# Performance work log

Measured on AMD Instinct MI355X. Metric: run time of the kernel, lower is better.

The kernel has to match this reference:

```python
import jax, jax.numpy as jnp
import numpy as np


def _layernorm(x, g, b, eps=1e-5):
    m = x.mean(-1, keepdims=True)
    v = ((x - m) ** 2).mean(-1, keepdims=True)
    return (x - m) / jnp.sqrt(v + eps) * g + b


def _rotate_every_two(x):
    x1 = x[..., ::2]
    x2 = x[..., 1::2]
    return jnp.stack([-x2, x1], axis=-1).reshape(x.shape)


def _segsum(x):
    # x: (..., L) of negative decay rates -> (..., L, L) bidirectional segment sums
    cs = jnp.cumsum(x, axis=-1)
    d = cs[..., :, None] - cs[..., None, :]
    L = x.shape[-1]
    i = jnp.arange(L)[:, None]
    j = jnp.arange(L)[None, :]
    # lower-tri (incl diag): cs[i]-cs[j]; strict upper: cs[j]-cs[i]; diag is 0
    return jnp.where(i >= j, d, -d)


def _forward(x, y, th, dw1_w, dw1_b, dw2_w, dw2_b, qw, qb, kw, kb, vw, vb,
             lepe_w, lepe_b, dt_w, dt_bias, A_log, ow, ob,
             n1_g, n1_b, ffn_w1, ffn_b1, ffn_w2, ffn_b2, n2_g, n2_b):
    B, C, H, W = x.shape
    nh = dt_bias.shape[0]
    hd = C // nh
    scaling = hd ** (-0.5)

    # dynamic gated fusion of the two kv branches (1x1 convs == channel matmuls)
    fusion = jnp.concatenate([y, th], axis=1)                      # (B,2C,H,W)
    hid = jax.nn.relu(jnp.einsum('bchw,oc->bohw', fusion, dw1_w) + dw1_b[None, :, None, None])
    logits = jnp.einsum('bchw,oc->bohw', hid, dw2_w) + dw2_b[None, :, None, None]
    wts = jax.nn.softmax(logits, axis=1)                           # (B,2,H,W)
    fused = y * wts[:, 0:1] + th * wts[:, 1:2]

    xh = jnp.transpose(x, (0, 2, 3, 1))                            # (B,H,W,C)
    fkv = jnp.transpose(fused, (0, 2, 3, 1))

    # 2D RoPE tables (flattened raster index)
    angle = jnp.repeat(1.0 / 10000 ** jnp.linspace(0.0, 1.0, hd // 2), 2)
    idx = jnp.arange(H * W, dtype=x.dtype)
    sin = jnp.sin(idx[:, None] * angle[None, :]).reshape(H, W, hd)
    cos = jnp.cos(idx[:, None] * angle[None, :]).reshape(H, W, hd)

    q = xh @ qw + qb
    k = fkv @ kw + kb
    v = fkv @ vw + vb

    # depthwise 5x5 conv position term on v (NHWC)
    lepe = jax.lax.conv_general_dilated(
        v, lepe_w, (1, 1), ((2, 2), (2, 2)),
        dimension_numbers=('NHWC', 'HWIO', 'NHWC'), feature_group_count=C) + lepe_b

    k = k * scaling
    q = q.reshape(B, H, W, nh, hd).transpose(0, 3, 1, 2, 4)        # (B,nh,H,W,hd)
    k = k.reshape(B, H, W, nh, hd).transpose(0, 3, 1, 2, 4)
    v5 = v.reshape(B, H, W, nh, hd).transpose(0, 3, 1, 2, 4)

    qr = q * cos + _rotate_every_two(q) * sin
    kr = k * cos + _rotate_every_two(k) * sin

    # PathEmbeding2D: data-dependent decay masks
    xt = xh.reshape(B, H * W, nh, hd)
    dt = xt @ dt_w                                                 # (B,S,nh,2)
    A = -jnp.exp(A_log)                                            # (nh,)
    da = jax.nn.softplus(dt[..., 0] + dt_bias) * A                 # (B,S,nh)
    db = jax.nn.softplus(dt[..., 1] + dt_bias) * A
    mask_w = _segsum(da.reshape(B, H, W, nh).transpose(0, 1, 3, 2))  # (B,H,nh,W,W)
    mask_h = _segsum(db.reshape(B, H, W, nh).transpose(0, 2, 3, 1))  # (B,W,nh,H,H)

    # row (width-direction) and column (height-direction) attentions
    qk_w = jax.nn.softmax(jnp.einsum('bnhid,bnhjd->bhnij', qr, kr) + mask_w, axis=-1)  # (B,H,nh,W,W)
    qk_h = jax.nn.softmax(jnp.einsum('bnhwd,bngwd->bwnhg', qr, kr) + mask_h, axis=-1)  # (B,W,nh,H,H)

    v_w = jnp.einsum('bhnij,bnhjd->bhnid', qk_w, v5)               # (B,H,nh,W,hd)
    out1 = jnp.einsum('bwnhg,bgnwd->bwnhd', qk_h, v_w)             # (B,W,nh,H,hd)
    out1 = out1.transpose(0, 3, 1, 2, 4).reshape(B, H, W, C)

    v_h = jnp.einsum('bwnhg,bngwd->bwnhd', qk_h, v5)               # (B,W,nh,H,hd)
    out2 = jnp.einsum('bhnij,bjnhd->bhnid', qk_w, v_h)             # (B,H,nh,W,hd)
    out2 = out2.transpose(0, 1, 3, 2, 4).reshape(B, H, W, C)

    out = 0.5 * out1 + 0.5 * out2 + lepe
    out = out @ ow + ob
    out = _layernorm(xh + out, n1_g, n1_b)
    ffn = jax.nn.gelu(out @ ffn_w1 + ffn_b1, approximate=False) @ ffn_w2 + ffn_b2
    out = _layernorm(out + ffn, n2_g, n2_b)
    return jnp.transpose(out, (0, 3, 1, 2))                        # (B,C,H,W)


def setup_inputs() -> dict:
    B, C, H, W, nh = 4, 64, 128, 128, 4
    hd = C // nh
    key = jax.random.key(0)
    ks = jax.random.split(key, 20)
    n = lambda k, shp, s: jax.random.normal(k, shp, dtype=jnp.float32) * s
    rng = np.random.default_rng(0)
    dt = np.exp(rng.uniform(0.0, 1.0, nh) * (np.log(0.1) - np.log(0.001)) + np.log(0.001))
    dt = np.clip(dt, 1e-4, None)
    dt_bias = jnp.asarray(dt + np.log(-np.expm1(-dt)), dtype=jnp.float32)
    A_log = jnp.asarray(np.log(rng.uniform(1.0, 1.1, nh)), dtype=jnp.float32)
    inp = {
        'x': n(ks[0], (B, C, H, W), 1.0),
        'y': n(ks[1], (B, C, H, W), 1.0),
        'th': n(ks[2], (B, C, H, W), 1.0),
        'dw1_w': n(ks[3], (C, 2 * C), (2 * C) ** -0.5),
        'dw1_b': jnp.zeros((C,), jnp.float32),
        'dw2_w': n(ks[4], (2, C), C ** -0.5),
        'dw2_b': jnp.zeros((2,), jnp.float32),
        'qw': n(ks[5], (C, C), 0.2 * C ** -0.5),
        'qb': jnp.zeros((C,), jnp.float32),
        'kw': n(ks[6], (C, C), 0.2 * C ** -0.5),
        'kb': jnp.zeros((C,), jnp.float32),
        'vw': n(ks[7], (C, C), 0.2 * C ** -0.5),
        'vb': jnp.zeros((C,), jnp.float32),
        'lepe_w': n(ks[8], (5, 5, 1, C), 0.1),
        'lepe_b': jnp.zeros((C,), jnp.float32),
        'dt_w': n(ks[9], (hd, 2), hd ** -0.5),
        'dt_bias': dt_bias,
        'A_log': A_log,
        'ow': n(ks[10], (C, C), C ** -0.5),
        'ob': jnp.zeros((C,), jnp.float32),
        'n1_g': jnp.ones((C,), jnp.float32),
        'n1_b': jnp.zeros((C,), jnp.float32),
        'ffn_w1': n(ks[11], (C, 4 * C), C ** -0.5),
        'ffn_b1': jnp.zeros((4 * C,), jnp.float32),
        'ffn_w2': n(ks[12], (4 * C, C), (4 * C) ** -0.5),
        'ffn_b2': jnp.zeros((C,), jnp.float32),
        'n2_g': jnp.ones((C,), jnp.float32),
        'n2_b': jnp.zeros((C,), jnp.float32),
    }
    return inp


def reference(x, y, th, dw1_w, dw1_b, dw2_w, dw2_b, qw, qb, kw, kb, vw, vb,
              lepe_w, lepe_b, dt_w, dt_bias, A_log, ow, ob,
              n1_g, n1_b, ffn_w1, ffn_b1, ffn_w2, ffn_b2, n2_g, n2_b):
    return _forward(x, y, th, dw1_w, dw1_b, dw2_w, dw2_b, qw, qb, kw, kb, vw, vb,
                    lepe_w, lepe_b, dt_w, dt_bias, A_log, ow, ob,
                    n1_g, n1_b, ffn_w1, ffn_b1, ffn_w2, ffn_b2, n2_g, n2_b)
```

## Files before the change

kernel.cpp:

```cpp
#include <hip/hip_runtime.h>
#include <math.h>

#define HWSZ 16384

typedef __attribute__((ext_vector_type(8))) short bf16x8;
typedef __attribute__((ext_vector_type(4))) float f32x4;
typedef unsigned short u16;

union U4 { uint4 v; u16 s[8]; };
union U2 { uint2 v; u16 s[4]; };

__device__ __forceinline__ float gelu_f(float v) {
    return 0.5f * v * (1.0f + erff(v * 0.70710678118654752f));
}
__device__ __forceinline__ float splus_f(float v) {
    return (v > 20.f) ? v : log1pf(expf(v));
}
__device__ __forceinline__ u16 f2bf(float f) {
    union { float f; unsigned u; } v; v.f = f;
    unsigned r = (v.u + 0x7FFF + ((v.u >> 16) & 1)) >> 16;
    return (u16)r;
}
__device__ __forceinline__ unsigned pk2(float a, float b) {
    return (unsigned)f2bf(a) | ((unsigned)f2bf(b) << 16);
}
__device__ __forceinline__ float bf2f(u16 s) {
    union { unsigned u; float f; } v; v.u = ((unsigned)s) << 16; return v.f;
}

__global__ __launch_bounds__(256) void k_prep(
    const float* __restrict__ w1, const float* __restrict__ qw,
    const float* __restrict__ kw, const float* __restrict__ vw,
    const float* __restrict__ ow, const float* __restrict__ fw1s,
    const float* __restrict__ fw2s, u16* __restrict__ wout)
{
    int id = blockIdx.x*256 + threadIdx.x;
    float v;
    if (id < 8192) {
        v = w1[id];
    } else if (id < 20480) {
        int t = id - 8192; int m = t >> 12;
        int i = t & 4095; int o = i >> 6, c = i & 63;
        const float* src = (m==0) ? qw : ((m==1) ? kw : vw);
        v = src[c*64 + o];
        if (m == 1) v *= 0.25f;
    } else if (id < 24576) {
        int i = id - 20480; int c = i >> 6, k = i & 63;
        v = ow[k*64 + c];
    } else if (id < 40960) {
        int i = id - 24576; int o = i >> 6, k = i & 63;
        v = fw1s[k*256 + o];
    } else {
        int i = id - 40960; int jc = i >> 12; int r = i & 4095;
        int c = r >> 6, k2 = r & 63;
        v = fw2s[(jc*64 + k2)*64 + c];
    }
    wout[id] = f2bf(v);
}

#define FS 136
__global__ __launch_bounds__(256) void k_fuse(
    const float* __restrict__ y, const float* __restrict__ th,
    const u16* __restrict__ wfuse, const float* __restrict__ b1,
    const float* __restrict__ w2, const float* __restrict__ b2,
    u16* __restrict__ fused)
{
    __shared__ u16 Fsh[128*FS];
    __shared__ u16 Wt[64*FS];
    int tid = threadIdx.x, bid = blockIdx.x;
    int pbase = bid*128;
    int b = pbase >> 14, p0 = pbase & 16383;
    for (int vi = tid; vi < 1024; vi += 256) {
        int cp = vi >> 5;
        int p4 = (vi & 31)*4;
        int c0 = cp*2;
        float4 a = *(const float4*)&y [((size_t)(b*64+c0  ))*HWSZ + p0 + p4];
        float4 c = *(const float4*)&y [((size_t)(b*64+c0+1))*HWSZ + p0 + p4];
        *(unsigned*)&Fsh[(p4+0)*FS + c0] = pk2(a.x, c.x);
        *(unsigned*)&Fsh[(p4+1)*FS + c0] = pk2(a.y, c.y);
        *(unsigned*)&Fsh[(p4+2)*FS + c0] = pk2(a.z, c.z);
        *(unsigned*)&Fsh[(p4+3)*FS + c0] = pk2(a.w, c.w);
        float4 e = *(const float4*)&th[((size_t)(b*64+c0  ))*HWSZ + p0 + p4];
        float4 f = *(const float4*)&th[((size_t)(b*64+c0+1))*HWSZ + p0 + p4];
        *(unsigned*)&Fsh[(p4+0)*FS + 64 + c0] = pk2(e.x, f.x);
        *(unsigned*)&Fsh[(p4+1)*FS + 64 + c0] = pk2(e.y, f.y);
        *(unsigned*)&Fsh[(p4+2)*FS + 64 + c0] = pk2(e.z, f.z);
        *(unsigned*)&Fsh[(p4+3)*FS + 64 + c0] = pk2(e.w, f.w);
    }
    for (int vi = tid; vi < 1024; vi += 256) {
        int o = vi >> 4, s8 = (vi & 15)*8;
        *(uint4*)&Wt[o*FS + s8] = *(const uint4*)&wfuse[o*128 + s8];
    }
    __syncthreads();
    int lane = tid & 63, wv = tid >> 6;
    int quad = lane >> 4, lm = lane & 15;
    int M0 = wv*32;
    f32x4 z = {0.f,0.f,0.f,0.f};
    f32x4 acc[2][4];
    #pragma unroll
    for (int mt = 0; mt < 2; ++mt)
        #pragma unroll
        for (int nt = 0; nt < 4; ++nt) acc[mt][nt] = z;
    #pragma unroll
    for (int ks = 0; ks < 4; ++ks) {
        bf16x8 aF[2];
        #pragma unroll
        for (int mt = 0; mt < 2; ++mt)
            aF[mt] = *(bf16x8*)&Fsh[(M0+mt*16+lm)*FS + ks*32 + quad*8];
        #pragma unroll
        for (int nt = 0; nt < 4; ++nt) {
            bf16x8 bW = *(bf16x8*)&Wt[(nt*16+lm)*FS + ks*32 + quad*8];
            #pragma unroll
            for (int mt = 0; mt < 2; ++mt)
                acc[mt][nt] = __builtin_amdgcn_mfma_f32_16x16x32_bf16(aF[mt], bW, acc[mt][nt], 0,0,0);
        }
    }
    float b1v[4], w2av[4], w2bv[4];
    #pragma unroll
    for (int nt = 0; nt < 4; ++nt) {
        int o = nt*16 + lm;
        b1v[nt] = b1[o]; w2av[nt] = w2[o]; w2bv[nt] = w2[64+o];
    }
    float bias2a = b2[0], bias2b = b2[1];
    size_t gbase = (size_t)(b*16384 + p0);
    #pragma unroll
    for (int mt = 0; mt < 2; ++mt) {
        #pragma unroll
        for (int r = 0; r < 4; ++r) {
            int p = M0 + mt*16 + quad*4 + r;
            float l0 = 0.f, l1 = 0.f;
            #pragma unroll
            for (int nt = 0; nt < 4; ++nt) {
                float h = fmaxf(acc[mt][nt][r] + b1v[nt], 0.f);
                l0 += h * w2av[nt];
                l1 += h * w2bv[nt];
            }
            l0 += __shfl_xor(l0,1,64); l0 += __shfl_xor(l0,2,64);
            l0 += __shfl_xor(l0,4,64); l0 += __shfl_xor(l0,8,64);
            l1 += __shfl_xor(l1,1,64); l1 += __shfl_xor(l1,2,64);
            l1 += __shfl_xor(l1,4,64); l1 += __shfl_xor(l1,8,64);
            l0 += bias2a; l1 += bias2b;
            float m = fmaxf(l0, l1);
            float e0 = __expf(l0 - m), e1 = __expf(l1 - m);
            float inv = 1.f/(e0 + e1);
            float wa = e0*inv, wb = e1*inv;
            U2 yv, tv;
            yv.v = *(uint2*)&Fsh[p*FS + lm*4];
            tv.v = *(uint2*)&Fsh[p*FS + 64 + lm*4];
            unsigned o0 = pk2(bf2f(yv.s[0])*wa + bf2f(tv.s[0])*wb,
                              bf2f(yv.s[1])*wa + bf2f(tv.s[1])*wb);
            unsigned o1 = pk2(bf2f(yv.s[2])*wa + bf2f(tv.s[2])*wb,
                              bf2f(yv.s[3])*wa + bf2f(tv.s[3])*wb);
            *(uint2*)&fused[(gbase + p)*64 + lm*4] = make_uint2(o0, o1);
        }
    }
}

__global__ __launch_bounds__(256) void k_qkv(
    const float* __restrict__ x, const u16* __restrict__ fused,
    const u16* __restrict__ bq, const float* __restrict__ qb,
    const u16* __restrict__ bk, const float* __restrict__ kb,
    const u16* __restrict__ bv, const float* __restrict__ vb,
    const float* __restrict__ dtw, const float* __restrict__ dtb,
    const float* __restrict__ alog,
    u16* __restrict__ qr, u16* __restrict__ kr, u16* __restrict__ v5,
    float* __restrict__ da, float* __restrict__ db)
{
    __shared__ u16 Ax[64*72];
    __shared__ u16 Af[64*72];
    __shared__ u16 Bq[64*72], Bk[64*72], Bv[64*72];
    int tid = threadIdx.x, bid = blockIdx.x;
    int pbase = bid*64;
    int b = pbase >> 14, p0 = pbase & 16383;
    for (int vi = tid; vi < 512; vi += 256) {
        int cp = vi >> 4, p4 = (vi & 15)*4;
        int c0 = cp*2;
        float4 a = *(const float4*)&x[((size_t)(b*64+c0  ))*HWSZ + p0 + p4];
        float4 c = *(const float4*)&x[((size_t)(b*64+c0+1))*HWSZ + p0 + p4];
        *(unsigned*)&Ax[(p4+0)*72 + c0] = pk2(a.x, c.x);
        *(unsigned*)&Ax[(p4+1)*72 + c0] = pk2(a.y, c.y);
        *(unsigned*)&Ax[(p4+2)*72 + c0] = pk2(a.z, c.z);
        *(unsigned*)&Ax[(p4+3)*72 + c0] = pk2(a.w, c.w);
    }
    for (int vi = tid; vi < 512; vi += 256) {
        int p = vi >> 3, seg = (vi & 7)*8;
        *(uint4*)&Af[p*72 + seg] = *(const uint4*)&fused[((size_t)(b*16384) + p0 + p)*64 + seg];
    }
    for (int vi = tid; vi < 1536; vi += 256) {
        int m = vi >> 9;
        int i = vi & 511;
        int o = i >> 3, s8 = (i & 7)*8;
        const u16* src = (m==0) ? bq : ((m==1) ? bk : bv);
        u16* dst = (m==0) ? Bq : ((m==1) ? Bk : Bv);
        *(uint4*)&dst[o*72 + s8] = *(const uint4*)&src[o*64 + s8];
    }
    __syncthreads();
    int lane = tid & 63, wv = tid >> 6;
    int quad = lane >> 4, lm = lane & 15;
    int M0 = wv*16;
    f32x4 z = {0.f,0.f,0.f,0.f};
    f32x4 accQ[4], accK[4], accV[4];
    #pragma unroll
    for (int nt = 0; nt < 4; ++nt) { accQ[nt]=z; accK[nt]=z; accV[nt]=z; }
    #pragma unroll
    for (int ks = 0; ks < 2; ++ks) {
        bf16x8 aX = *(bf16x8*)&Ax[(M0+lm)*72 + ks*32 + quad*8];
        bf16x8 aF = *(bf16x8*)&Af[(M0+lm)*72 + ks*32 + quad*8];
        #pragma unroll
        for (int nt = 0; nt < 4; ++nt) {
            bf16x8 bQ = *(bf16x8*)&Bq[(nt*16+lm)*72 + ks*32 + quad*8];
            bf16x8 bK = *(bf16x8*)&Bk[(nt*16+lm)*72 + ks*32 + quad*8];
            bf16x8 bV = *(bf16x8*)&Bv[(nt*16+lm)*72 + ks*32 + quad*8];
            accQ[nt] = __builtin_amdgcn_mfma_f32_16x16x32_bf16(aX, bQ, accQ[nt], 0,0,0);
            accK[nt] = __builtin_amdgcn_mfma_f32_16x16x32_bf16(aF, bK, accK[nt], 0,0,0);
            accV[nt] = __builtin_amdgcn_mfma_f32_16x16x32_bf16(aF, bV, accV[nt], 0,0,0);
        }
    }
    {
        float dtw_[32];
        #pragma unroll
        for (int i = 0; i < 32; ++i) dtw_[i] = dtw[i];
        int p = tid >> 2, n = tid & 3;
        U4 a, c;
        a.v = *(const uint4*)&Ax[p*72 + n*16];
        c.v = *(const uint4*)&Ax[p*72 + n*16 + 8];
        float dt0 = 0.f, dt1 = 0.f;
        #pragma unroll
        for (int d = 0; d < 8; ++d) {
            float xv = bf2f(a.s[d]);
            dt0 += xv*dtw_[2*d];
            dt1 += xv*dtw_[2*d+1];
        }
        #pragma unroll
        for (int d = 0; d < 8; ++d) {
            float xv = bf2f(c.s[d]);
            dt0 += xv*dtw_[16+2*d];
            dt1 += xv*dtw_[16+2*d+1];
        }
        float A = -expf(alog[n]);
        float bb = dtb[n];
        int P = p0 + p;
        int h = P >> 7, w = P & 127;
        da[((b*128+h)*4+n)*128 + w] = splus_f(dt0+bb)*A;
        db[((b*128+w)*4+n)*128 + h] = splus_f(dt1+bb)*A;
    }
    float qbv[4], kbv[4], vbv[4];
    #pragma unroll
    for (int nt = 0; nt < 4; ++nt) {
        qbv[nt] = qb[nt*16+lm]; kbv[nt] = kb[nt*16+lm]*0.25f; vbv[nt] = vb[nt*16+lm];
    }
    bool evn = !(lm & 1);
    float ang = exp2f(-1.89824462565f * (float)(lm >> 1));
    int bb4 = b*4;
    #pragma unroll
    for (int r = 0; r < 4; ++r) {
        int P = p0 + M0 + quad*4 + r;
        float sn_, cs_;
        sincosf((float)P * ang, &sn_, &cs_);
        #pragma unroll
        for (int nt = 0; nt < 4; ++nt) {
            float vq = accQ[nt][r] + qbv[nt];
            float pq = __shfl_xor(vq, 1, 64);
            float rq = evn ? vq*cs_ - pq*sn_ : vq*cs_ + pq*sn_;
            unsigned uq = f2bf(rq);
            unsigned upq = (unsigned)__shfl_xor((int)uq, 1, 64);
            float vk = accK[nt][r] + kbv[nt];
            float pk = __shfl_xor(vk, 1, 64);
            float rk = evn ? vk*cs_ - pk*sn_ : vk*cs_ + pk*sn_;
            unsigned uk = f2bf(rk);
            unsigned upk = (unsigned)__shfl_xor((int)uk, 1, 64);
            unsigned uv = f2bf(accV[nt][r] + vbv[nt]);
            unsigned upv = (unsigned)__shfl_xor((int)uv, 1, 64);
            if (evn) {
                size_t off = ((size_t)(bb4+nt)*HWSZ + P)*16 + lm;
                *(unsigned*)&qr[off] = (uq & 0xffff) | (upq << 16);
                *(unsigned*)&kr[off] = (uk & 0xffff) | (upk << 16);
                *(unsigned*)&v5[off] = (uv & 0xffff) | (upv << 16);
            }
        }
    }
}

#define LROW 328
__global__ __launch_bounds__(256) void k_lepe(
    const u16* __restrict__ v5, const float* __restrict__ lw,
    const float* __restrict__ lb, u16* __restrict__ lepe)
{
    __shared__ float sv[36*LROW];
    __shared__ float swt[400];
    int tid = threadIdx.x, bid = blockIdx.x;
    int tw = bid & 7, th_ = (bid >> 3) & 3, n = (bid >> 5) & 3, b = bid >> 7;
    int bn = b*4 + n;
    int h0 = th_*32, w0 = tw*16;
    for (int i = tid; i < 400; i += 256) {
        int tap = i >> 4, d = i & 15;
        swt[i] = lw[tap*64 + n*16 + d];
    }
    const u16* vb = v5 + (size_t)bn*HWSZ*16;
    for (int vi = tid; vi < 1440; vi += 256) {
        int cell = vi >> 1, half = vi & 1;
        int hh = cell/20, ww = cell - hh*20;
        int h = h0 - 2 + hh, w = w0 - 2 + ww;
        U4 val; val.v = make_uint4(0,0,0,0);
        if (h >= 0 && h < 128 && w >= 0 && w < 128)
            val.v = *(const uint4*)&vb[((size_t)(h*128+w))*16 + half*8];
        float* dst = &sv[hh*LROW + ww*16 + half*8];
        #pragma unroll
        for (int u = 0; u < 8; ++u) dst[u] = bf2f(val.s[u]);
    }
    __syncthreads();
    int df = (tid & 3)*4;
    int s  = tid >> 2;
    int ph = s >> 1;
    int pw = (s & 1)*8;
    float4 bv = *(const float4*)&lb[n*16 + df];
    float acc[8][4];
    #pragma unroll
    for (int ow = 0; ow < 8; ++ow) {
        acc[ow][0] = bv.x; acc[ow][1] = bv.y; acc[ow][2] = bv.z; acc[ow][3] = bv.w;
    }
    #pragma unroll
    for (int ky = 0; ky < 5; ++ky) {
        float wgt[5][4];
        #pragma unroll
        for (int kx = 0; kx < 5; ++kx) {
            float4 wv = *(const float4*)&swt[(ky*5+kx)*16 + df];
            wgt[kx][0]=wv.x; wgt[kx][1]=wv.y; wgt[kx][2]=wv.z; wgt[kx][3]=wv.w;
        }
        float dat[13][4];
        #pragma unroll
        for (int c = 0; c < 13; ++c) {
            float4 dv = *(const float4*)&sv[(ph+ky)*LROW + (pw+c)*16 + df];
            dat[c][0]=dv.x; dat[c][1]=dv.y; dat[c][2]=dv.z; dat[c][3]=dv.w;
        }
        #pragma unroll
        for (int ow = 0; ow < 8; ++ow)
            #pragma unroll
            for (int kx = 0; kx < 5; ++kx)
                #pragma unroll
                for (int u = 0; u < 4; ++u)
                    acc[ow][u] += dat[ow+kx][u]*wgt[kx][u];
    }
    u16* ob = lepe + ((size_t)bn*HWSZ + (size_t)(h0+ph)*128 + w0+pw)*16 + df;
    #pragma unroll
    for (int ow = 0; ow < 8; ++ow)
        *(uint2*)&ob[ow*16] = make_uint2(pk2(acc[ow][0],acc[ow][1]), pk2(acc[ow][2],acc[ow][3]));
}

__global__ __launch_bounds__(256) void k_attn_w1(
    const u16* __restrict__ qr, const u16* __restrict__ kr,
    const u16* __restrict__ v5, const float* __restrict__ dacs,
    u16* __restrict__ vwb)
{
    __shared__ u16 Vt[16*136], Ps[128*136];
    __shared__ float csr[128];
    int tid = threadIdx.x, bid = blockIdx.x;
    int h = bid & 127, n = (bid >> 7) & 3, b = bid >> 9;
    size_t rowoff = ((size_t)((b*4+n)*128 + h)) * 2048;
    {
        int jp = tid >> 2, q4 = tid & 3;
        U2 a, c;
        a.v = *(const uint2*)&v5[rowoff + (2*jp)*16 + q4*4];
        c.v = *(const uint2*)&v5[rowoff + (2*jp+1)*16 + q4*4];
        #pragma unroll
        for (int u = 0; u < 4; ++u)
            *(unsigned*)&Vt[(q4*4+u)*136 + 2*jp] = (unsigned)a.s[u] | ((unsigned)c.s[u] << 16);
    }
    if (tid < 128) csr[tid] = dacs[((b*128+h)*4+n)*128 + tid];
    __syncthreads();
    if (tid < 64) {
        float2 e = *(float2*)&csr[tid*2];
        float s = e.x + e.y;
        #pragma unroll
        for (int d = 1; d < 64; d <<= 1) {
            float t = __shfl_up(s, d, 64);
            if (tid >= d) s += t;
        }
        csr[tid*2]   = s - e.y;
        csr[tid*2+1] = s;
    }
    __syncthreads();
    int lane = tid & 63, wv = tid >> 6;
    int quad = lane >> 4, lm = lane & 15;
    int r0 = wv*32, r1 = wv*32 + 16;
    bf16x8 z8 = {0,0,0,0,0,0,0,0};
    bf16x8 aQ0 = z8, aQ1 = z8;
    if (quad < 2) {
        aQ0 = *(const bf16x8*)&qr[rowoff + (size_t)(r0+lm)*16 + quad*8];
        aQ1 = *(const bf16x8*)&qr[rowoff + (size_t)(r1+lm)*16 + quad*8];
    }
    float csj[8], csi0[4], csi1[4];
    #pragma unroll
    for (int jt = 0; jt < 8; ++jt) csj[jt] = csr[jt*16+lm];
    #pragma unroll
    for (int r = 0; r < 4; ++r) { csi0[r] = csr[r0+quad*4+r]; csi1[r] = csr[r1+quad*4+r]; }
    float ls0[4]={0,0,0,0}, ls1[4]={0,0,0,0};
    f32x4 z = {0.f,0.f,0.f,0.f};
    #pragma unroll
    for (int jt = 0; jt < 8; ++jt) {
        bf16x8 bK = z8;
        if (quad < 2) bK = *(const bf16x8*)&kr[rowoff + (size_t)(jt*16+lm)*16 + quad*8];
        f32x4 s0 = __builtin_amdgcn_mfma_f32_16x16x32_bf16(aQ0, bK, z, 0,0,0);
        f32x4 s1 = __builtin_amdgcn_mfma_f32_16x16x32_bf16(aQ1, bK, z, 0,0,0);
        #pragma unroll
        for (int r = 0; r < 4; ++r) {
            float e0 = __expf(s0[r] - fabsf(csi0[r]-csj[jt])); ls0[r] += e0;
            float e1 = __expf(s1[r] - fabsf(csi1[r]-csj[jt])); ls1[r] += e1;
            Ps[(r0+quad*4+r)*136 + jt*16+lm] = f2bf(e0);
            Ps[(r1+quad*4+r)*136 + jt*16+lm] = f2bf(e1);
        }
    }
    float inv0[4], inv1[4];
    #pragma unroll
    for (int r = 0; r < 4; ++r) {
        #pragma unroll
        for (int m = 1; m < 16; m <<= 1) {
            ls0[r] += __shfl_xor(ls0[r], m, 64);
            ls1[r] += __shfl_xor(ls1[r], m, 64);
        }
        inv0[r] = 1.f/ls0[r]; inv1[r] = 1.f/ls1[r];
    }
    __syncthreads();
    f32x4 acc0 = z, acc1 = z;
    #pragma unroll
    for (int c = 0; c < 4; ++c) {
        bf16x8 bV  = *(bf16x8*)&Vt[lm*136 + c*32 + quad*8];
        bf16x8 aP0 = *(bf16x8*)&Ps[(r0+lm)*136 + c*32 + quad*8];
        bf16x8 aP1 = *(bf16x8*)&Ps[(r1+lm)*136 + c*32 + quad*8];
        acc0 = __builtin_amdgcn_mfma_f32_16x16x32_bf16(aP0, bV, acc0, 0,0,0);
        acc1 = __builtin_amdgcn_mfma_f32_16x16x32_bf16(aP1, bV, acc1, 0,0,0);
    }
    bool evn = !(lm & 1);
    #pragma unroll
    for (int r = 0; r < 4; ++r) {
        int i0 = r0+quad*4+r, i1 = r1+quad*4+r;
        unsigned u0 = f2bf(acc0[r]*inv0[r]);
        unsigned u1 = f2bf(acc1[r]*inv1[r]);
        unsigned up0 = (unsigned)__shfl_xor((int)u0, 1, 64);
        unsigned up1 = (unsigned)__shfl_xor((int)u1, 1, 64);
        if (evn) {
            *(unsigned*)&vwb[rowoff + (size_t)i0*16 + lm] = (u0 & 0xffff) | (up0 << 16);
            *(unsigned*)&vwb[rowoff + (size_t)i1*16 + lm] = (u1 & 0xffff) | (up1 << 16);
        }
    }
}

__global__ __launch_bounds__(256) void k_attn_h(
    const u16* __restrict__ qr, const u16* __restrict__ kr,
    const u16* __restrict__ v5, const u16* __restrict__ vwb,
    const float* __restrict__ dbcs,
    u16* __restrict__ vhb, u16* __restrict__ o1b)
{
    __shared__ u16 Vt[16*136], Wt[16*136], Ps[128*136];
    __shared__ float csr[128];
    int tid = threadIdx.x, bid = blockIdx.x;
    int w = bid & 127, n = (bid >> 7) & 3, b = bid >> 9;
    int bn = b*4 + n;
    size_t base = ((size_t)bn*16384 + w)*16;
    {
        int jp = tid >> 2, q4 = tid & 3;
        U2 a, c, e, f;
        a.v = *(const uint2*)&v5 [base + (size_t)(2*jp)*2048 + q4*4];
        c.v = *(const uint2*)&v5 [base + (size_t)(2*jp+1)*2048 + q4*4];
        e.v = *(const uint2*)&vwb[base + (size_t)(2*jp)*2048 + q4*4];
        f.v = *(const uint2*)&vwb[base + (size_t)(2*jp+1)*2048 + q4*4];
        #pragma unroll
        for (int u = 0; u < 4; ++u) {
            *(unsigned*)&Vt[(q4*4+u)*136 + 2*jp] = (unsigned)a.s[u] | ((unsigned)c.s[u] << 16);
            *(unsigned*)&Wt[(q4*4+u)*136 + 2*jp] = (unsigned)e.s[u] | ((unsigned)f.s[u] << 16);
        }
    }
    if (tid < 128) csr[tid] = dbcs[((b*128+w)*4+n)*128 + tid];
    __syncthreads();
    if (tid < 64) {
        float2 e = *(float2*)&csr[tid*2];
        float s = e.x + e.y;
        #pragma unroll
        for (int d = 1; d < 64; d <<= 1) {
            float t = __shfl_up(s, d, 64);
            if (tid >= d) s += t;
        }
        csr[tid*2]   = s - e.y;
        csr[tid*2+1] = s;
    }
    __syncthreads();
    int lane = tid & 63, wv = tid >> 6;
    int quad = lane >> 4, lm = lane & 15;
    int r0 = wv*32, r1 = wv*32 + 16;
    bf16x8 z8 = {0,0,0,0,0,0,0,0};
    bf16x8 aQ0 = z8, aQ1 = z8;
    if (quad < 2) {
        aQ0 = *(const bf16x8*)&qr[base + (size_t)(r0+lm)*2048 + quad*8];
        aQ1 = *(const bf16x8*)&qr[base + (size_t)(r1+lm)*2048 + quad*8];
    }
    float csj[8], csi0[4], csi1[4];
    #pragma unroll
    for (int jt = 0; jt < 8; ++jt) csj[jt] = csr[jt*16+lm];
    #pragma unroll
    for (int r = 0; r < 4; ++r) { csi0[r] = csr[r0+quad*4+r]; csi1[r] = csr[r1+quad*4+r]; }
    float ls0[4]={0,0,0,0}, ls1[4]={0,0,0,0};
    f32x4 z = {0.f,0.f,0.f,0.f};
    #pragma unroll
    for (int jt = 0; jt < 8; ++jt) {
        bf16x8 bK = z8;
        if (quad < 2) bK = *(const bf16x8*)&kr[base + (size_t)(jt*16+lm)*2048 + quad*8];
        f32x4 s0 = __builtin_amdgcn_mfma_f32_16x16x32_bf16(aQ0, bK, z, 0,0,0);
        f32x4 s1 = __builtin_amdgcn_mfma_f32_16x16x32_bf16(aQ1, bK, z, 0,0,0);
        #pragma unroll
        for (int r = 0; r < 4; ++r) {
            float e0 = __expf(s0[r] - fabsf(csi0[r]-csj[jt])); ls0[r] += e0;
            float e1 = __expf(s1[r] - fabsf(csi1[r]-csj[jt])); ls1[r] += e1;
            Ps[(r0+quad*4+r)*136 + jt*16+lm] = f2bf(e0);
            Ps[(r1+quad*4+r)*136 + jt*16+lm] = f2bf(e1);
        }
    }
    float inv0[4], inv1[4];
    #pragma unroll
    for (int r = 0; r < 4; ++r) {
        #pragma unroll
        for (int m = 1; m < 16; m <<= 1) {
            ls0[r] += __shfl_xor(ls0[r], m, 64);
            ls1[r] += __shfl_xor(ls1[r], m, 64);
        }
        inv0[r] = 1.f/ls0[r]; inv1[r] = 1.f/ls1[r];
    }
    __syncthreads();
    f32x4 aV0 = z, aV1 = z, aW0 = z, aW1 = z;
    #pragma unroll
    for (int c = 0; c < 4; ++c) {
        bf16x8 bV  = *(bf16x8*)&Vt[lm*136 + c*32 + quad*8];
        bf16x8 bW  = *(bf16x8*)&Wt[lm*136 + c*32 + quad*8];
        bf16x8 aP0 = *(bf16x8*)&Ps[(r0+lm)*136 + c*32 + quad*8];
        bf16x8 aP1 = *(bf16x8*)&Ps[(r1+lm)*136 + c*32 + quad*8];
        aV0 = __builtin_amdgcn_mfma_f32_16x16x32_bf16(aP0, bV, aV0, 0,0,0);
        aV1 = __builtin_amdgcn_mfma_f32_16x16x32_bf16(aP1, bV, aV1, 0,0,0);
        aW0 = __builtin_amdgcn_mfma_f32_16x16x32_bf16(aP0, bW, aW0, 0,0,0);
        aW1 = __builtin_amdgcn_mfma_f32_16x16x32_bf16(aP1, bW, aW1, 0,0,0);
    }
    size_t obase = ((size_t)bn*16384 + (size_t)w*128)*16;
    bool evn = !(lm & 1);
    #pragma unroll
    for (int r = 0; r < 4; ++r) {
        int i0 = r0+quad*4+r, i1 = r1+quad*4+r;
        float v0 = inv0[r], v1 = inv1[r];
        unsigned a0 = f2bf(aV0[r]*v0), a1 = f2bf(aV1[r]*v1);
        unsigned b0 = f2bf(aW0[r]*v0), b1 = f2bf(aW1[r]*v1);
        unsigned ap0 = (unsigned)__shfl_xor((int)a0,1,64), ap1 = (unsigned)__shfl_xor((int)a1,1,64);
        unsigned bp0 = (unsigned)__shfl_xor((int)b0,1,64), bp1 = (unsigned)__shfl_xor((int)b1,1,64);
        if (evn) {
            *(unsigned*)&vhb[obase + (size_t)i0*16 + lm] = (a0 & 0xffff) | (ap0 << 16);
            *(unsigned*)&vhb[obase + (size_t)i1*16 + lm] = (a1 & 0xffff) | (ap1 << 16);
            *(unsigned*)&o1b[obase + (size_t)i0*16 + lm] = (b0 & 0xffff) | (bp0 << 16);
            *(unsigned*)&o1b[obase + (size_t)i1*16 + lm] = (b1 & 0xffff) | (bp1 << 16);
        }
    }
}

__global__ __launch_bounds__(256) void k_attn_w2(
    const u16* __restrict__ qr, const u16* __restrict__ kr,
    const u16* __restrict__ vhb, const u16* __restrict__ o1b,
    const float* __restrict__ dacs, const u16* __restrict__ lepe,
    u16* __restrict__ attn)
{
    __shared__ u16 Vt[16*136], Ps[128*136];
    __shared__ float csr[128];
    int tid = threadIdx.x, bid = blockIdx.x;
    int h = bid & 127, n = (bid >> 7) & 3, b = bid >> 9;
    int bn = b*4 + n;
    size_t rowoff = ((size_t)(bn*128 + h)) * 2048;
    size_t vbase  = (size_t)bn*262144 + (size_t)h*16;
    {
        int jp = tid >> 2, q4 = tid & 3;
        U2 a, c;
        a.v = *(const uint2*)&vhb[vbase + (size_t)(2*jp)*2048 + q4*4];
        c.v = *(const uint2*)&vhb[vbase + (size_t)(2*jp+1)*2048 + q4*4];
        #pragma unroll
        for (int u = 0; u < 4; ++u)
            *(unsigned*)&Vt[(q4*4+u)*136 + 2*jp] = (unsigned)a.s[u] | ((unsigned)c.s[u] << 16);
    }
    if (tid < 128) csr[tid] = dacs[((b*128+h)*4+n)*128 + tid];
    __syncthreads();
    if (tid < 64) {
        float2 e = *(float2*)&csr[tid*2];
        float s = e.x + e.y;
        #pragma unroll
        for (int d = 1; d < 64; d <<= 1) {
            float t = __shfl_up(s, d, 64);
            if (tid >= d) s += t;
        }
        csr[tid*2]   = s - e.y;
        csr[tid*2+1] = s;
    }
    __syncthreads();
    int lane = tid & 63, wv = tid >> 6;
    int quad = lane >> 4, lm = lane & 15;
    int r0 = wv*32, r1 = wv*32 + 16;
    bf16x8 z8 = {0,0,0,0,0,0,0,0};
    bf16x8 aQ0 = z8, aQ1 = z8;
    if (quad < 2) {
        aQ0 = *(const bf16x8*)&qr[rowoff + (size_t)(r0+lm)*16 + quad*8];
        aQ1 = *(const bf16x8*)&qr[rowoff + (size_t)(r1+lm)*16 + quad*8];
    }
    float csj[8], csi0[4], csi1[4];
    #pragma unroll
    for (int jt = 0; jt < 8; ++jt) csj[jt] = csr[jt*16+lm];
    #pragma unroll
    for (int r = 0; r < 4; ++r) { csi0[r] = csr[r0+quad*4+r]; csi1[r] = csr[r1+quad*4+r]; }
    float ls0[4]={0,0,0,0}, ls1[4]={0,0,0,0};
    f32x4 z = {0.f,0.f,0.f,0.f};
    #pragma unroll
    for (int jt = 0; jt < 8; ++jt) {
        bf16x8 bK = z8;
        if (quad < 2) bK = *(const bf16x8*)&kr[rowoff + (size_t)(jt*16+lm)*16 + quad*8];
        f32x4 s0 = __builtin_amdgcn_mfma_f32_16x16x32_bf16(aQ0, bK, z, 0,0,0);
        f32x4 s1 = __builtin_amdgcn_mfma_f32_16x16x32_bf16(aQ1, bK, z, 0,0,0);
        #pragma unroll
        for (int r = 0; r < 4; ++r) {
            float e0 = __expf(s0[r] - fabsf(csi0[r]-csj[jt])); ls0[r] += e0;
            float e1 = __expf(s1[r] - fabsf(csi1[r]-csj[jt])); ls1[r] += e1;
            Ps[(r0+quad*4+r)*136 + jt*16+lm] = f2bf(e0);
            Ps[(r1+quad*4+r)*136 + jt*16+lm] = f2bf(e1);
        }
    }
    float inv0[4], inv1[4];
    #pragma unroll
    for (int r = 0; r < 4; ++r) {
        #pragma unroll
        for (int m = 1; m < 16; m <<= 1) {
            ls0[r] += __shfl_xor(ls0[r], m, 64);
            ls1[r] += __shfl_xor(ls1[r], m, 64);
        }
        inv0[r] = 1.f/ls0[r]; inv1[r] = 1.f/ls1[r];
    }
    __syncthreads();
    f32x4 acc0 = z, acc1 = z;
    #pragma unroll
    for (int c = 0; c < 4; ++c) {
        bf16x8 bV  = *(bf16x8*)&Vt[lm*136 + c*32 + quad*8];
        bf16x8 aP0 = *(bf16x8*)&Ps[(r0+lm)*136 + c*32 + quad*8];
        bf16x8 aP1 = *(bf16x8*)&Ps[(r1+lm)*136 + c*32 + quad*8];
        acc0 = __builtin_amdgcn_mfma_f32_16x16x32_bf16(aP0, bV, acc0, 0,0,0);
        acc1 = __builtin_amdgcn_mfma_f32_16x16x32_bf16(aP1, bV, acc1, 0,0,0);
    }
    size_t lpb = (size_t)bn*262144 + (size_t)h*2048;
    size_t oab = (size_t)b*1048576 + (size_t)h*8192 + n*16;
    bool evn = !(lm & 1);
    #pragma unroll
    for (int r = 0; r < 4; ++r) {
        int i0 = r0+quad*4+r, i1 = r1+quad*4+r;
        float o2a = acc0[r]*inv0[r];
        float o2b = acc1[r]*inv1[r];
        float o1a = bf2f(o1b[vbase + (size_t)i0*2048 + lm]);
        float o1c = bf2f(o1b[vbase + (size_t)i1*2048 + lm]);
        float la  = bf2f(lepe[lpb + (size_t)i0*16 + lm]);
        float lc  = bf2f(lepe[lpb + (size_t)i1*16 + lm]);
        unsigned ua = f2bf(0.5f*(o1a + o2a) + la);
        unsigned uc = f2bf(0.5f*(o1c + o2b) + lc);
        unsigned upa = (unsigned)__shfl_xor((int)ua,1,64);
        unsigned upc = (unsigned)__shfl_xor((int)uc,1,64);
        if (evn) {
            *(unsigned*)&attn[oab + (size_t)i0*64 + lm] = (ua & 0xffff) | (upa << 16);
            *(unsigned*)&attn[oab + (size_t)i1*64 + lm] = (uc & 0xffff) | (upc << 16);
        }
    }
}

__global__ __launch_bounds__(256) void k_proj_ln(
    const u16* __restrict__ attn, const float* __restrict__ x,
    const u16* __restrict__ bo, const float* __restrict__ ob,
    const float* __restrict__ g1, const float* __restrict__ b1,
    u16* __restrict__ t1)
{
    __shared__ u16 As[64*72];
    __shared__ u16 Bs[64*72];
    __shared__ float XT[64*68];
    int tid = threadIdx.x, bid = blockIdx.x;
    int pbase = bid*64;
    int b = pbase >> 14, p0 = pbase & 16383;
    for (int vi = tid; vi < 512; vi += 256) {
        int p = vi >> 3, s8 = (vi & 7)*8;
        *(uint4*)&As[p*72 + s8] = *(const uint4*)&attn[((size_t)(pbase+p))*64 + s8];
    }
    for (int vi = tid; vi < 512; vi += 256) {
        int c = vi >> 3, s8 = (vi & 7)*8;
        *(uint4*)&Bs[c*72 + s8] = *(const uint4*)&bo[c*64 + s8];
    }
    for (int vi = tid; vi < 1024; vi += 256) {
        int c = vi >> 4, p4 = (vi & 15)*4;
        *(float4*)&XT[c*68 + p4] = *(const float4*)&x[((size_t)(b*64+c))*HWSZ + p0 + p4];
    }
    __syncthreads();
    int lane = tid & 63, wv = tid >> 6;
    int quad = lane >> 4, lm = lane & 15;
    int M0 = wv*16;
    float xv[4][4], obv[4], g1v[4], b1v[4];
    #pragma unroll
    for (int nt = 0; nt < 4; ++nt) {
        int c = nt*16 + lm;
        obv[nt] = ob[c]; g1v[nt] = g1[c]; b1v[nt] = b1[c];
        #pragma unroll
        for (int r = 0; r < 4; ++r)
            xv[nt][r] = XT[c*68 + M0 + quad*4 + r];
    }
    f32x4 z = {0.f,0.f,0.f,0.f};
    f32x4 acc[4];
    #pragma unroll
    for (int nt = 0; nt < 4; ++nt) acc[nt] = z;
    #pragma unroll
    for (int ks = 0; ks < 2; ++ks) {
        bf16x8 aF = *(bf16x8*)&As[(M0+lm)*72 + ks*32 + quad*8];
        #pragma unroll
        for (int nt = 0; nt < 4; ++nt) {
            bf16x8 bF = *(bf16x8*)&Bs[(nt*16+lm)*72 + ks*32 + quad*8];
            acc[nt] = __builtin_amdgcn_mfma_f32_16x16x32_bf16(aF, bF, acc[nt], 0,0,0);
        }
    }
    float val[4][4], res[4][4];
    #pragma unroll
    for (int r = 0; r < 4; ++r) {
        float s = 0.f;
        #pragma unroll
        for (int nt = 0; nt < 4; ++nt) {
            val[nt][r] = acc[nt][r] + obv[nt] + xv[nt][r];
            s += val[nt][r];
        }
        s += __shfl_xor(s, 1, 64); s += __shfl_xor(s, 2, 64);
        s += __shfl_xor(s, 4, 64); s += __shfl_xor(s, 8, 64);
        float mean = s*(1.f/64.f);
        float vv = 0.f;
        #pragma unroll
        for (int nt = 0; nt < 4; ++nt) {
            float d = val[nt][r] - mean;
            vv += d*d;
        }
        vv += __shfl_xor(vv, 1, 64); vv += __shfl_xor(vv, 2, 64);
        vv += __shfl_xor(vv, 4, 64); vv += __shfl_xor(vv, 8, 64);
        float rs = rsqrtf(vv*(1.f/64.f) + 1e-5f);
        #pragma unroll
        for (int nt = 0; nt < 4; ++nt)
            res[nt][r] = (val[nt][r] - mean)*rs*g1v[nt] + b1v[nt];
    }
    __syncthreads();
    float* outT = XT;
    #pragma unroll
    for (int r = 0; r < 4; ++r)
        #pragma unroll
        for (int nt = 0; nt < 4; ++nt)
            outT[(M0+quad*4+r)*68 + nt*16 + lm] = res[nt][r];
    __syncthreads();
    for (int vi = tid; vi < 512; vi += 256) {
        int p = vi >> 3, s8 = (vi & 7)*8;
        float4 f0 = *(const float4*)&outT[p*68 + s8];
        float4 f1 = *(const float4*)&outT[p*68 + s8 + 4];
        uint4 o = make_uint4(pk2(f0.x,f0.y), pk2(f0.z,f0.w), pk2(f1.x,f1.y), pk2(f1.z,f1.w));
        *(uint4*)&t1[((size_t)(pbase+p))*64 + s8] = o;
    }
}

__global__ __launch_bounds__(256) void k_ffn(
    const u16* __restrict__ t1, const u16* __restrict__ fw1,
    const float* __restrict__ b1f, const u16* __restrict__ fw2,
    const float* __restrict__ b2f, const float* __restrict__ g2,
    const float* __restrict__ bb2, float* __restrict__ outp)
{
    __shared__ u16 SL[18432];
    __shared__ float sb1[256];
    __shared__ float sb2[64], sg[64], sbb[64];
    u16* At1 = SL;
    u16* W1b = SL + 4608;
    u16* W2b = SL + 9216;
    u16* Hid = SL + 13824;
    int tid = threadIdx.x, bid = blockIdx.x;
    int pbase = bid*64;
    int b = pbase >> 14, p0 = pbase & 16383;
    for (int vi = tid; vi < 512; vi += 256) {
        int p = vi >> 3, s8 = (vi & 7)*8;
        *(uint4*)&At1[p*72 + s8] = *(const uint4*)&t1[((size_t)(pbase+p))*64 + s8];
    }
    if (tid < 256) sb1[tid] = b1f[tid];
    if (tid < 64) { sb2[tid] = b2f[tid]; sg[tid] = g2[tid]; sbb[tid] = bb2[tid]; }
    int lane = tid & 63, wv = tid >> 6;
    int quad = lane >> 4, lm = lane & 15;
    int M0 = wv*16;
    f32x4 z = {0.f,0.f,0.f,0.f};
    f32x4 acc2[4];
    #pragma unroll
    for (int nt = 0; nt < 4; ++nt) acc2[nt] = z;
    for (int jc = 0; jc < 4; ++jc) {
        __syncthreads();
        for (int vi = tid; vi < 1024; vi += 256) {
            int m = vi >> 9, i = vi & 511;
            int o = i >> 3, s8 = (i & 7)*8;
            if (m == 0) *(uint4*)&W1b[o*72 + s8] = *(const uint4*)&fw1[(jc*64+o)*64 + s8];
            else        *(uint4*)&W2b[o*72 + s8] = *(const uint4*)&fw2[jc*4096 + o*64 + s8];
        }
        __syncthreads();
        f32x4 h[4];
        #pragma unroll
        for (int nt = 0; nt < 4; ++nt) h[nt] = z;
        #pragma unroll
        for (int ks = 0; ks < 2; ++ks) {
            bf16x8 aF = *(bf16x8*)&At1[(M0+lm)*72 + ks*32 + quad*8];
            #pragma unroll
            for (int nt = 0; nt < 4; ++nt) {
                bf16x8 bF = *(bf16x8*)&W1b[(nt*16+lm)*72 + ks*32 + quad*8];
                h[nt] = __builtin_amdgcn_mfma_f32_16x16x32_bf16(aF, bF, h[nt], 0,0,0);
            }
        }
        #pragma unroll
        for (int nt = 0; nt < 4; ++nt) {
            float bb = sb1[jc*64 + nt*16 + lm];
            #pragma unroll
            for (int r = 0; r < 4; ++r) {
                float hv = gelu_f(h[nt][r] + bb);
                unsigned u = (unsigned)f2bf(hv);
                unsigned up = (unsigned)__shfl_xor((int)u, 1, 64);
                if (!(lm & 1))
                    *(unsigned*)&Hid[(M0+quad*4+r)*72 + nt*16 + lm] = (u & 0xffff) | (up << 16);
            }
        }
        #pragma unroll
        for (int ks = 0; ks < 2; ++ks) {
            bf16x8 aH = *(bf16x8*)&Hid[(M0+lm)*72 + ks*32 + quad*8];
            #pragma unroll
            for (int nt = 0; nt < 4; ++nt) {
                bf16x8 bF = *(bf16x8*)&W2b[(nt*16+lm)*72 + ks*32 + quad*8];
                acc2[nt] = __builtin_amdgcn_mfma_f32_16x16x32_bf16(aH, bF, acc2[nt], 0,0,0);
            }
        }
    }
    float val[4][4], res[4][4];
    float sb2v[4], sgv[4], sbbv[4];
    #pragma unroll
    for (int nt = 0; nt < 4; ++nt) {
        int c = nt*16 + lm;
        sb2v[nt] = sb2[c]; sgv[nt] = sg[c]; sbbv[nt] = sbb[c];
    }
    #pragma unroll
    for (int r = 0; r < 4; ++r) {
        int pos = M0 + quad*4 + r;
        float s = 0.f;
        #pragma unroll
        for (int nt = 0; nt < 4; ++nt) {
            float tv = bf2f(At1[pos*72 + nt*16 + lm]);
            val[nt][r] = acc2[nt][r] + sb2v[nt] + tv;
            s += val[nt][r];
        }
        s += __shfl_xor(s, 1, 64); s += __shfl_xor(s, 2, 64);
        s += __shfl_xor(s, 4, 64); s += __shfl_xor(s, 8, 64);
        float mean = s*(1.f/64.f);
        float vv = 0.f;
        #pragma unroll
        for (int nt = 0; nt < 4; ++nt) {
            float d = val[nt][r] - mean;
            vv += d*d;
        }
        vv += __shfl_xor(vv, 1, 64); vv += __shfl_xor(vv, 2, 64);
        vv += __shfl_xor(vv, 4, 64); vv += __shfl_xor(vv, 8, 64);
        float rs = rsqrtf(vv*(1.f/64.f) + 1e-5f);
        #pragma unroll
        for (int nt = 0; nt < 4; ++nt)
            res[nt][r] = (val[nt][r] - mean)*rs*sgv[nt] + sbbv[nt];
    }
    __syncthreads();
    float* outT = (float*)SL;
    #pragma unroll
    for (int r = 0; r < 4; ++r)
        #pragma unroll
        for (int nt = 0; nt < 4; ++nt)
            outT[(nt*16+lm)*68 + M0 + quad*4 + r] = res[nt][r];
    __syncthreads();
    for (int vi = tid; vi < 1024; vi += 256) {
        int c = vi >> 4, p4 = (vi & 15)*4;
        *(float4*)&outp[((size_t)(b*64+c))*HWSZ + p0 + p4] = *(const float4*)&outT[c*68 + p4];
    }
}

extern "C" void kernel_launch(void* const* d_in, const int* in_sizes, int n_in,
                              void* d_out, int out_size, void* d_ws, size_t ws_size,
                              hipStream_t stream) {
    const float* x      = (const float*)d_in[0];
    const float* y      = (const float*)d_in[1];
    const float* th     = (const float*)d_in[2];
    const float* dw1_w  = (const float*)d_in[3];
    const float* dw1_b  = (const float*)d_in[4];
    const float* dw2_w  = (const float*)d_in[5];
    const float* dw2_b  = (const float*)d_in[6];
    const float* qw     = (const float*)d_in[7];
    const float* qb     = (const float*)d_in[8];
    const float* kw     = (const float*)d_in[9];
    const float* kb     = (const float*)d_in[10];
    const float* vw     = (const float*)d_in[11];
    const float* vb     = (const float*)d_in[12];
    const float* lepe_w = (const float*)d_in[13];
    const float* lepe_b = (const float*)d_in[14];
    const float* dt_w   = (const float*)d_in[15];
    const float* dt_bias= (const float*)d_in[16];
    const float* A_log  = (const float*)d_in[17];
    const float* ow     = (const float*)d_in[18];
    const float* ob     = (const float*)d_in[19];
    const float* n1_g   = (const float*)d_in[20];
    const float* n1_b   = (const float*)d_in[21];
    const float* ffn_w1 = (const float*)d_in[22];
    const float* ffn_b1 = (const float*)d_in[23];
    const float* ffn_w2 = (const float*)d_in[24];
    const float* ffn_b2 = (const float*)d_in[25];
    const float* n2_g   = (const float*)d_in[26];
    const float* n2_b   = (const float*)d_in[27];
    float* out = (float*)d_out;

    const size_t SZ = 4194304;
    float* ws    = (float*)d_ws;
    u16* fused = (u16*)(ws + 0*SZ);
    u16* qrb   = (u16*)(ws + 1*SZ);
    u16* krb   = (u16*)(ws + 2*SZ);
    u16* v5b   = (u16*)(ws + 3*SZ);
    u16* lepeb = (u16*)(ws + 4*SZ);
    u16* vhb   = (u16*)(ws + 5*SZ);
    u16* o1b   = (u16*)(ws + 6*SZ);
    u16* attnb = (u16*)(ws + 7*SZ);
    u16* t1b   = (u16*)(ws + 8*SZ);
    float* dacs  = ws + 9*SZ;
    float* dbcs  = ws + 9*SZ + 262144;
    u16* wall  = (u16*)(ws + 9*SZ + 524288);
    u16* wfuse = wall;
    u16* bq    = wall + 8192;
    u16* bk    = wall + 12288;
    u16* bv    = wall + 16384;
    u16* bo    = wall + 20480;
    u16* fw1   = wall + 24576;
    u16* fw2   = wall + 40960;

    k_prep<<<224, 256, 0, stream>>>(dw1_w, qw, kw, vw, ow, ffn_w1, ffn_w2, wall);
    k_fuse<<<512, 256, 0, stream>>>(y, th, wfuse, dw1_b, dw2_w, dw2_b, fused);
    k_qkv<<<1024, 256, 0, stream>>>(x, fused, bq, qb, bk, kb, bv, vb,
                                    dt_w, dt_bias, A_log, qrb, krb, v5b, dacs, dbcs);
    k_lepe<<<512, 256, 0, stream>>>(v5b, lepe_w, lepe_b, lepeb);
    k_attn_w1<<<2048, 256, 0, stream>>>(qrb, krb, v5b, dacs, fused);
    k_attn_h<<<2048, 256, 0, stream>>>(qrb, krb, v5b, fused, dbcs, vhb, o1b);
    k_attn_w2<<<2048, 256, 0, stream>>>(qrb, krb, vhb, o1b, dacs, lepeb, attnb);
    k_proj_ln<<<1024, 256, 0, stream>>>(attnb, x, bo, ob, n1_g, n1_b, t1b);
    k_ffn<<<1024, 256, 0, stream>>>(t1b, fw1, ffn_b1, fw2, ffn_b2, n2_g, n2_b, out);
}
```

Before: 292.8 us.

## Fuse gated kv fusion kernel into QKV projection kernel via shared memory

Merges k_fuse and k_qkv into a single kernel that processes 64 pixels per block. The gated fused kv tile is computed and written straight to shared memory and consumed by the K/V projections, so the global round-trip of the fused bf16 tensor and one launch go away. Shared memory is aliased between phases to keep the footprint bounded. The trade-off is an extra barrier, halved M-tile per block for the fusion GEMM, and the fusion weight tile now being reloaded by twice as many blocks.

```diff
diff --git a/kernel.cpp b/kernel.cpp
--- a/kernel.cpp
+++ b/kernel.cpp
@@ -58,80 +58,84 @@
     wout[id] = f2bf(v);
 }
 
-#define FS 136
-__global__ __launch_bounds__(256) void k_fuse(
-    const float* __restrict__ y, const float* __restrict__ th,
+__global__ __launch_bounds__(256) void k_fuse_qkv(
+    const float* __restrict__ x, const float* __restrict__ y,
+    const float* __restrict__ th,
     const u16* __restrict__ wfuse, const float* __restrict__ b1,
     const float* __restrict__ w2, const float* __restrict__ b2,
-    u16* __restrict__ fused)
+    const u16* __restrict__ bq, const float* __restrict__ qb,
+    const u16* __restrict__ bk, const float* __restrict__ kb,
+    const u16* __restrict__ bv, const float* __restrict__ vb,
+    const float* __restrict__ dtw, const float* __restrict__ dtb,
+    const float* __restrict__ alog,
+    u16* __restrict__ qr, u16* __restrict__ kr, u16* __restrict__ v5,
+    float* __restrict__ da, float* __restrict__ db)
 {
-    __shared__ u16 Fsh[128*FS];
-    __shared__ u16 Wt[64*FS];
+    __shared__ u16 SL[18432];
+    __shared__ u16 AfL[4608];
+    u16* Fsh = SL;
+    u16* Wt  = SL + 8704;
+    u16* Ax  = SL;
+    u16* Bq  = SL + 4608;
+    u16* Bk  = SL + 9216;
+    u16* Bv  = SL + 13824;
+    u16* Af  = AfL;
     int tid = threadIdx.x, bid = blockIdx.x;
-    int pbase = bid*128;
+    int pbase = bid*64;
     int b = pbase >> 14, p0 = pbase & 16383;
-    for (int vi = tid; vi < 1024; vi += 256) {
-        int cp = vi >> 5;
-        int p4 = (vi & 31)*4;
+    int lane = tid & 63, wv = tid >> 6;
+    int quad = lane >> 4, lm = lane & 15;
+    int M0 = wv*16;
+    f32x4 z = {0.f,0.f,0.f,0.f};
+
+    for (int vi = tid; vi < 512; vi += 256) {
+        int cp = vi >> 4, p4 = (vi & 15)*4;
         int c0 = cp*2;
         float4 a = *(const float4*)&y [((size_t)(b*64+c0  ))*HWSZ + p0 + p4];
         float4 c = *(const float4*)&y [((size_t)(b*64+c0+1))*HWSZ + p0 + p4];
-        *(unsigned*)&Fsh[(p4+0)*FS + c0] = pk2(a.x, c.x);
-        *(unsigned*)&Fsh[(p4+1)*FS + c0] = pk2(a.y, c.y);
-        *(unsigned*)&Fsh[(p4+2)*FS + c0] = pk2(a.z, c.z);
-        *(unsigned*)&Fsh[(p4+3)*FS + c0] = pk2(a.w, c.w);
+        *(unsigned*)&Fsh[(p4+0)*136 + c0] = pk2(a.x, c.x);
+        *(unsigned*)&Fsh[(p4+1)*136 + c0] = pk2(a.y, c.y);
+        *(unsigned*)&Fsh[(p4+2)*136 + c0] = pk2(a.z, c.z);
+        *(unsigned*)&Fsh[(p4+3)*136 + c0] = pk2(a.w, c.w);
         float4 e = *(const float4*)&th[((size_t)(b*64+c0  ))*HWSZ + p0 + p4];
         float4 f = *(const float4*)&th[((size_t)(b*64+c0+1))*HWSZ + p0 + p4];
-        *(unsigned*)&Fsh[(p4+0)*FS + 64 + c0] = pk2(e.x, f.x);
-        *(unsigned*)&Fsh[(p4+1)*FS + 64 + c0] = pk2(e.y, f.y);
-        *(unsigned*)&Fsh[(p4+2)*FS + 64 + c0] = pk2(e.z, f.z);
-        *(unsigned*)&Fsh[(p4+3)*FS + 64 + c0] = pk2(e.w, f.w);
+        *(unsigned*)&Fsh[(p4+0)*136 + 64 + c0] = pk2(e.x, f.x);
+        *(unsigned*)&Fsh[(p4+1)*136 + 64 + c0] = pk2(e.y, f.y);
+        *(unsigned*)&Fsh[(p4+2)*136 + 64 + c0] = pk2(e.z, f.z);
+        *(unsigned*)&Fsh[(p4+3)*136 + 64 + c0] = pk2(e.w, f.w);
     }
     for (int vi = tid; vi < 1024; vi += 256) {
         int o = vi >> 4, s8 = (vi & 15)*8;
-        *(uint4*)&Wt[o*FS + s8] = *(const uint4*)&wfuse[o*128 + s8];
-    }
-    __syncthreads();
-    int lane = tid & 63, wv = tid >> 6;
-    int quad = lane >> 4, lm = lane & 15;
-    int M0 = wv*32;
-    f32x4 z = {0.f,0.f,0.f,0.f};
-    f32x4 acc[2][4];
-    #pragma unroll
-    for (int mt = 0; mt < 2; ++mt)
-        #pragma unroll
-        for (int nt = 0; nt < 4; ++nt) acc[mt][nt] = z;
-    #pragma unroll
-    for (int ks = 0; ks < 4; ++ks) {
-        bf16x8 aF[2];
-        #pragma unroll
-        for (int mt = 0; mt < 2; ++mt)
-            aF[mt] = *(bf16x8*)&Fsh[(M0+mt*16+lm)*FS + ks*32 + quad*8];
+        *(uint4*)&Wt[o*136 + s8] = *(const uint4*)&wfuse[o*128 + s8];
+    }
+    __syncthreads();
+    {
+        f32x4 acc[4];
+        #pragma unroll
+        for (int nt = 0; nt < 4; ++nt) acc[nt] = z;
+        #pragma unroll
+        for (int ks = 0; ks < 4; ++ks) {
+            bf16x8 aF = *(bf16x8*)&Fsh[(M0+lm)*136 + ks*32 + quad*8];
+            #pragma unroll
+            for (int nt = 0; nt < 4; ++nt) {
+                bf16x8 bW = *(bf16x8*)&Wt[(nt*16+lm)*136 + ks*32 + quad*8];
+                acc[nt] = __builtin_amdgcn_mfma_f32_16x16x32_bf16(aF, bW, acc[nt], 0,0,0);
+            }
+        }
+        float b1v[4], w2av[4], w2bv[4];
         #pragma unroll
         for (int nt = 0; nt < 4; ++nt) {
-            bf16x8 bW = *(bf16x8*)&Wt[(nt*16+lm)*FS + ks*32 + quad*8];
-            #pragma unroll
-            for (int mt = 0; mt < 2; ++mt)
-                acc[mt][nt] = __builtin_amdgcn_mfma_f32_16x16x32_bf16(aF[mt], bW, acc[mt][nt], 0,0,0);
-        }
-    }
-    float b1v[4], w2av[4], w2bv[4];
-    #pragma unroll
-    for (int nt = 0; nt < 4; ++nt) {
-        int o = nt*16 + lm;
-        b1v[nt] = b1[o]; w2av[nt] = w2[o]; w2bv[nt] = w2[64+o];
-    }
-    float bias2a = b2[0], bias2b = b2[1];
-    size_t gbase = (size_t)(b*16384 + p0);
-    #pragma unroll
-    for (int mt = 0; mt < 2; ++mt) {
+            int o = nt*16 + lm;
+            b1v[nt] = b1[o]; w2av[nt] = w2[o]; w2bv[nt] = w2[64+o];
+        }
+        float bias2a = b2[0], bias2b = b2[1];
         #pragma unroll
         for (int r = 0; r < 4; ++r) {
-            int p = M0 + mt*16 + quad*4 + r;
+            int p = M0 + quad*4 + r;
             float l0 = 0.f, l1 = 0.f;
             #pragma unroll
             for (int nt = 0; nt < 4; ++nt) {
-                float h = fmaxf(acc[mt][nt][r] + b1v[nt], 0.f);
+                float h = fmaxf(acc[nt][r] + b1v[nt], 0.f);
                 l0 += h * w2av[nt];
                 l1 += h * w2bv[nt];
             }
@@ -145,33 +149,17 @@
             float inv = 1.f/(e0 + e1);
             float wa = e0*inv, wb = e1*inv;
             U2 yv, tv;
-            yv.v = *(uint2*)&Fsh[p*FS + lm*4];
-            tv.v = *(uint2*)&Fsh[p*FS + 64 + lm*4];
+            yv.v = *(uint2*)&Fsh[p*136 + lm*4];
+            tv.v = *(uint2*)&Fsh[p*136 + 64 + lm*4];
             unsigned o0 = pk2(bf2f(yv.s[0])*wa + bf2f(tv.s[0])*wb,
                               bf2f(yv.s[1])*wa + bf2f(tv.s[1])*wb);
             unsigned o1 = pk2(bf2f(yv.s[2])*wa + bf2f(tv.s[2])*wb,
                               bf2f(yv.s[3])*wa + bf2f(tv.s[3])*wb);
-            *(uint2*)&fused[(gbase + p)*64 + lm*4] = make_uint2(o0, o1);
-        }
-    }
-}
-
-__global__ __launch_bounds__(256) void k_qkv(
-    const float* __restrict__ x, const u16* __restrict__ fused,
-    const u16* __restrict__ bq, const float* __restrict__ qb,
-    const u16* __restrict__ bk, const float* __restrict__ kb,
-    const u16* __restrict__ bv, const float* __restrict__ vb,
-    const float* __restrict__ dtw, const float* __restrict__ dtb,
-    const float* __restrict__ alog,
-    u16* __restrict__ qr, u16* __restrict__ kr, u16* __restrict__ v5,
-    float* __restrict__ da, float* __restrict__ db)
-{
-    __shared__ u16 Ax[64*72];
-    __shared__ u16 Af[64*72];
-    __shared__ u16 Bq[64*72], Bk[64*72], Bv[64*72];
-    int tid = threadIdx.x, bid = blockIdx.x;
-    int pbase = bid*64;
-    int b = pbase >> 14, p0 = pbase & 16383;
+            *(uint2*)&Af[p*72 + lm*4] = make_uint2(o0, o1);
+        }
+    }
+    __syncthreads();
+
     for (int vi = tid; vi < 512; vi += 256) {
         int cp = vi >> 4, p4 = (vi & 15)*4;
         int c0 = cp*2;
@@ -182,10 +170,6 @@
         *(unsigned*)&Ax[(p4+2)*72 + c0] = pk2(a.z, c.z);
         *(unsigned*)&Ax[(p4+3)*72 + c0] = pk2(a.w, c.w);
     }
-    for (int vi = tid; vi < 512; vi += 256) {
-        int p = vi >> 3, seg = (vi & 7)*8;
-        *(uint4*)&Af[p*72 + seg] = *(const uint4*)&fused[((size_t)(b*16384) + p0 + p)*64 + seg];
-    }
     for (int vi = tid; vi < 1536; vi += 256) {
         int m = vi >> 9;
         int i = vi & 511;
@@ -195,10 +179,6 @@
         *(uint4*)&dst[o*72 + s8] = *(const uint4*)&src[o*64 + s8];
     }
     __syncthreads();
-    int lane = tid & 63, wv = tid >> 6;
-    int quad = lane >> 4, lm = lane & 15;
-    int M0 = wv*16;
-    f32x4 z = {0.f,0.f,0.f,0.f};
     f32x4 accQ[4], accK[4], accV[4];
     #pragma unroll
     for (int nt = 0; nt < 4; ++nt) { accQ[nt]=z; accK[nt]=z; accV[nt]=z; }
@@ -911,7 +891,7 @@
 
     const size_t SZ = 4194304;
     float* ws    = (float*)d_ws;
-    u16* fused = (u16*)(ws + 0*SZ);
+    u16* vwbuf = (u16*)(ws + 0*SZ);
     u16* qrb   = (u16*)(ws + 1*SZ);
     u16* krb   = (u16*)(ws + 2*SZ);
     u16* v5b   = (u16*)(ws + 3*SZ);
@@ -932,12 +912,12 @@
     u16* fw2   = wall + 40960;
 
     k_prep<<<224, 256, 0, stream>>>(dw1_w, qw, kw, vw, ow, ffn_w1, ffn_w2, wall);
-    k_fuse<<<512, 256, 0, stream>>>(y, th, wfuse, dw1_b, dw2_w, dw2_b, fused);
-    k_qkv<<<1024, 256, 0, stream>>>(x, fused, bq, qb, bk, kb, bv, vb,
-                                    dt_w, dt_bias, A_log, qrb, krb, v5b, dacs, dbcs);
+    k_fuse_qkv<<<1024, 256, 0, stream>>>(x, y, th, wfuse, dw1_b, dw2_w, dw2_b,
+                                         bq, qb, bk, kb, bv, vb,
+                                         dt_w, dt_bias, A_log, qrb, krb, v5b, dacs, dbcs);
     k_lepe<<<512, 256, 0, stream>>>(v5b, lepe_w, lepe_b, lepeb);
-    k_attn_w1<<<2048, 256, 0, stream>>>(qrb, krb, v5b, dacs, fused);
-    k_attn_h<<<2048, 256, 0, stream>>>(qrb, krb, v5b, fused, dbcs, vhb, o1b);
+    k_attn_w1<<<2048, 256, 0, stream>>>(qrb, krb, v5b, dacs, vwbuf);
+    k_attn_h<<<2048, 256, 0, stream>>>(qrb, krb, v5b, vwbuf, dbcs, vhb, o1b);
     k_attn_w2<<<2048, 256, 0, stream>>>(qrb, krb, vhb, o1b, dacs, lepeb, attnb);
     k_proj_ln<<<1024, 256, 0, stream>>>(attnb, x, bo, ob, n1_g, n1_b, t1b);
     k_ffn<<<1024, 256, 0, stream>>>(t1b, fw1, ffn_b1, fw2, ffn_b2, n2_g, n2_b, out);
```

New measurement: 300.0 us. 1.02x slower.
